# Kernel optimization log

Hardware: AMD Instinct MI355X
Metric: run time of the kernel (lower is better)

Reference implementation:

```python
import jax, jax.numpy as jnp
import numpy as np

N, T, D_FEAT, H = 8192, 60, 6, 64
NEG_SLOPE = 0.01  # torch LeakyReLU default


def setup_inputs() -> dict:
    key = jax.random.key(0)
    ks = jax.random.split(key, 20)
    s = lambda k, shape, fan: jax.random.normal(k, shape, jnp.float32) * (1.0 / np.sqrt(fan))
    inp = {
        'x': jax.random.normal(ks[0], (N, T, D_FEAT), jnp.float32),
        # LSTM layer 0 (input D_FEAT) and layer 1 (input H); gate order i,f,g,o
        'Wih0': s(ks[1], (4 * H, D_FEAT), H), 'Whh0': s(ks[2], (4 * H, H), H),
        'bih0': s(ks[3], (4 * H,), H), 'bhh0': s(ks[4], (4 * H,), H),
        'Wih1': s(ks[5], (4 * H, H), H), 'Whh1': s(ks[6], (4 * H, H), H),
        'bih1': s(ks[7], (4 * H,), H), 'bhh1': s(ks[8], (4 * H,), H),
        # GAT layer: transformation Linear(H,H) and attention vector a [2H,1] (randn in torch)
        'Wt': s(ks[9], (H, H), H), 'bt': s(ks[10], (H,), H),
        'a': jax.random.normal(ks[11], (2 * H, 1), jnp.float32),
        # fc and fc_out
        'Wfc': s(ks[12], (H, H), H), 'bfc': s(ks[13], (H,), H),
        'Wout': s(ks[14], (1, H), H), 'bout': s(ks[15], (1,), H),
    }
    return inp


def _lstm_layer(x, Wih, Whh, bih, bhh):
    # x: [N, T, Din] -> outputs [N, T, H]
    xg = jnp.einsum('ntd,gd->ntg', x, Wih) + bih + bhh  # precompute input gates

    def step(carry, xt):
        h, c = carry
        gates = xt + h @ Whh.T  # [N, 4H]
        i, f, g, o = jnp.split(gates, 4, axis=-1)
        c = jax.nn.sigmoid(f) * c + jax.nn.sigmoid(i) * jnp.tanh(g)
        h = jax.nn.sigmoid(o) * jnp.tanh(c)
        return (h, c), h

    n = x.shape[0]
    h0 = jnp.zeros((n, Whh.shape[1]), x.dtype)
    (_, _), hs = jax.lax.scan(step, (h0, h0), jnp.swapaxes(xg, 0, 1))
    return jnp.swapaxes(hs, 0, 1)


def _gat_layer(x, Wt, bt, a):
    # att[i,j] = leaky_relu(a1 . Wx_j + a2 . Wx_i); softmax over j; out = att @ x
    h = x @ Wt.T + bt                    # [N, H]
    hdim = h.shape[1]
    s1 = (h @ a[:hdim]).squeeze(-1)      # a1 . Wx_j  -> column term
    s2 = (h @ a[hdim:]).squeeze(-1)      # a2 . Wx_i  -> row term
    scores = jax.nn.leaky_relu(s2[:, None] + s1[None, :], NEG_SLOPE)  # [N, N]
    att = jax.nn.softmax(scores, axis=1)
    return att @ x


def reference(x, Wih0, Whh0, bih0, bhh0, Wih1, Whh1, bih1, bhh1,
              Wt, bt, a, Wfc, bfc, Wout, bout):
    out = _lstm_layer(x, Wih0, Whh0, bih0, bhh0)
    out = _lstm_layer(out, Wih1, Whh1, bih1, bhh1)
    last = out[:, -1, :]                 # [N, H]
    hidden = _gat_layer(last, Wt, bt, a) + last  # num_layers_gat = 1
    hidden = jax.nn.leaky_relu(hidden @ Wfc.T + bfc, NEG_SLOPE)
    return (hidden @ Wout.T + bout).squeeze(-1)  # [N]
```

## Files before the change

### kernel.cpp

```cpp
#include <hip/hip_runtime.h>

#define NN 8192
#define TT 60
#define DF 6
#define HH 64
#define GG 256
#define RS 132
#define CH 32
#define NB 256

typedef _Float16 half8 __attribute__((ext_vector_type(8)));
typedef float f32x4 __attribute__((ext_vector_type(4)));
#define MFMA16(a, b, c) __builtin_amdgcn_mfma_f32_16x16x32_f16((a), (b), (c), 0, 0, 0)

#define LOG2E 1.44269504f

__device__ __forceinline__ float lrelu_(float x) { return x > 0.0f ? x : 0.01f * x; }

__device__ __forceinline__ float lstm_act2(float gi, float gf, float gg, float go,
                                           float& c)
{
    const float ei = __builtin_amdgcn_exp2f(gi * -LOG2E);
    const float ef = __builtin_amdgcn_exp2f(gf * -LOG2E);
    const float eg = __builtin_amdgcn_exp2f(fminf(gg * (-2.f * LOG2E), 63.f));
    const float sf = __builtin_amdgcn_rcpf(1.f + ef);
    const float tg_si = (1.f - eg) * __builtin_amdgcn_rcpf((1.f + ei) * (1.f + eg));
    c = __builtin_fmaf(sf, c, tg_si);
    const float eo = __builtin_amdgcn_exp2f(go * -LOG2E);
    const float ec = __builtin_amdgcn_exp2f(fminf(c * (-2.f * LOG2E), 63.f));
    return (1.f - ec) * __builtin_amdgcn_rcpf((1.f + eo) * (1.f + ec));
}

__device__ __forceinline__ half8 ldw8(const float* __restrict__ p) {
    const float4* q = (const float4*)p;
    float4 u = q[0], v = q[1];
    half8 r;
    r[0]=(_Float16)u.x; r[1]=(_Float16)u.y; r[2]=(_Float16)u.z; r[3]=(_Float16)u.w;
    r[4]=(_Float16)v.x; r[5]=(_Float16)v.y; r[6]=(_Float16)v.z; r[7]=(_Float16)v.w;
    return r;
}

#define SXW (TT * 8 + 8)

__global__ __launch_bounds__(512, 4)
void lstm_fused_kernel(const float* __restrict__ x,
                       const float* __restrict__ Wih0, const float* __restrict__ Whh0,
                       const float* __restrict__ bih0, const float* __restrict__ bhh0,
                       const float* __restrict__ Wih1, const float* __restrict__ Whh1,
                       const float* __restrict__ bih1, const float* __restrict__ bhh1,
                       const float* __restrict__ Wt, const float* __restrict__ bt,
                       const float* __restrict__ av,
                       float* __restrict__ last_out,
                       float* __restrict__ s1g, float* __restrict__ s2g)
{
    __shared__ _Float16 sxp[16][SXW];
    __shared__ _Float16 h0buf[2][16][72];
    __shared__ _Float16 h1buf[2][16][72];
    __shared__ _Float16 zero16[8];
    __shared__ float sv1[HH], sv2[HH], sc12[2];

    const int tid  = threadIdx.x;
    const int w    = tid >> 6;
    const int grp  = w >> 2;
    const int cg   = w & 3;
    const int lane = tid & 63;
    const int quad = lane >> 4;
    const int l15  = lane & 15;
    const int hc   = cg * 16 + l15;
    const int n0   = blockIdx.x * 16;

    for (int i = tid; i < 16 * SXW / 2; i += 512) ((unsigned*)sxp)[i] = 0u;
    for (int i = tid; i < 2 * 16 * 72 / 2; i += 512) ((unsigned*)h0buf)[i] = 0u;
    for (int i = tid; i < 2 * 16 * 72 / 2; i += 512) ((unsigned*)h1buf)[i] = 0u;
    if (tid < 4) ((unsigned*)zero16)[tid] = 0u;
    __syncthreads();

    for (int idx = tid; idx < 16 * TT * DF; idx += 512) {
        const int m = idx / (TT * DF);
        const int r = idx - m * (TT * DF);
        const int t = r / DF;
        const int d = r - t * DF;
        sxp[m][t * 8 + d] = (_Float16)x[(size_t)(n0 + m) * (TT * DF) + r];
    }

    if (tid < HH) {
        float a1 = 0.f, a2 = 0.f;
        #pragma unroll 8
        for (int h = 0; h < HH; h++) {
            const float wt = Wt[h * HH + tid];
            a1 += wt * av[h];
            a2 += wt * av[HH + h];
        }
        sv1[tid] = a1; sv2[tid] = a2;
    } else if (tid == 64 || tid == 65) {
        const float* ap = av + (tid - 64) * HH;
        float c = 0.f;
        #pragma unroll 8
        for (int h = 0; h < HH; h++) c += bt[h] * ap[h];
        sc12[tid - 64] = c;
    }

    half8 wA[4][2], wB[4][2];
    float bias[4];
    half8 hzero;
    #pragma unroll
    for (int j = 0; j < 8; j++) hzero[j] = (_Float16)0.f;

    if (grp == 0) {
        #pragma unroll
        for (int nt = 0; nt < 4; nt++) {
            const int g = nt * 64 + hc;
            wA[nt][0] = ldw8(Whh0 + (size_t)g * HH + quad * 8);
            wA[nt][1] = ldw8(Whh0 + (size_t)g * HH + 32 + quad * 8);
            bias[nt]  = bih0[g] + bhh0[g];
            half8 t = hzero;
            if (quad == 0) {
                #pragma unroll
                for (int j = 0; j < DF; j++) t[j] = (_Float16)Wih0[g * DF + j];
            }
            wB[nt][0] = t;
            wB[nt][1] = hzero;
        }
    } else {
        #pragma unroll
        for (int nt = 0; nt < 4; nt++) {
            const int g = nt * 64 + hc;
            wA[nt][0] = ldw8(Wih1 + (size_t)g * HH + quad * 8);
            wA[nt][1] = ldw8(Wih1 + (size_t)g * HH + 32 + quad * 8);
            wB[nt][0] = ldw8(Whh1 + (size_t)g * HH + quad * 8);
            wB[nt][1] = ldw8(Whh1 + (size_t)g * HH + 32 + quad * 8);
            bias[nt]  = bih1[g] + bhh1[g];
        }
    }

    float cs[4] = {0.f, 0.f, 0.f, 0.f};
    __syncthreads();

    for (int i = 0; i <= TT; i++) {
        const int p = i & 1;
        if (grp == 0) {
            if (i < TT) {
                const half8 a0 = *(const half8*)&h0buf[p][l15][quad * 8];
                const half8 a1 = *(const half8*)&h0buf[p][l15][32 + quad * 8];
                const _Float16* xap = (quad == 0) ? &sxp[l15][i * 8] : zero16;
                const half8 ax = *(const half8*)xap;
                f32x4 gv[4];
                #pragma unroll
                for (int nt = 0; nt < 4; nt++) {
                    f32x4 c; c[0] = bias[nt]; c[1] = bias[nt]; c[2] = bias[nt]; c[3] = bias[nt];
                    c = MFMA16(ax, wB[nt][0], c);
                    c = MFMA16(a0, wA[nt][0], c);
                    c = MFMA16(a1, wA[nt][1], c);
                    gv[nt] = c;
                }
                _Float16 (*h0w)[72] = h0buf[p ^ 1];
                #pragma unroll
                for (int reg = 0; reg < 4; reg++) {
                    const float hv = lstm_act2(gv[0][reg], gv[1][reg], gv[2][reg], gv[3][reg], cs[reg]);
                    h0w[quad * 4 + reg][hc] = (_Float16)hv;
                }
            }
        } else {
            if (i > 0) {
                const half8 a00 = *(const half8*)&h0buf[p][l15][quad * 8];
                const half8 a01 = *(const half8*)&h0buf[p][l15][32 + quad * 8];
                const half8 a10 = *(const half8*)&h1buf[p][l15][quad * 8];
                const half8 a11 = *(const half8*)&h1buf[p][l15][32 + quad * 8];
                f32x4 gv[4];
                #pragma unroll
                for (int nt = 0; nt < 4; nt++) {
                    f32x4 c; c[0] = bias[nt]; c[1] = bias[nt]; c[2] = bias[nt]; c[3] = bias[nt];
                    c = MFMA16(a00, wA[nt][0], c);
                    c = MFMA16(a01, wA[nt][1], c);
                    c = MFMA16(a10, wB[nt][0], c);
                    c = MFMA16(a11, wB[nt][1], c);
                    gv[nt] = c;
                }
                _Float16 (*h1w)[72] = h1buf[p ^ 1];
                #pragma unroll
                for (int reg = 0; reg < 4; reg++) {
                    const float hv = lstm_act2(gv[0][reg], gv[1][reg], gv[2][reg], gv[3][reg], cs[reg]);
                    h1w[quad * 4 + reg][hc] = (_Float16)hv;
                    if (i == TT) last_out[(size_t)(n0 + quad * 4 + reg) * HH + hc] = hv;
                }
            }
        }
        __syncthreads();
    }

    {
        const _Float16 (*hf)[72] = h1buf[1];
        const int r  = tid >> 5;
        const int c0 = tid & 31;
        const float h1a = (float)hf[r][c0];
        const float h1b = (float)hf[r][c0 + 32];
        float p1 = h1a * sv1[c0] + h1b * sv1[c0 + 32];
        float p2 = h1a * sv2[c0] + h1b * sv2[c0 + 32];
        #pragma unroll
        for (int off = 16; off > 0; off >>= 1) {
            p1 += __shfl_xor(p1, off);
            p2 += __shfl_xor(p2, off);
        }
        if (c0 == 0) {
            s1g[n0 + r] = p1 + sc12[0];
            s2g[n0 + r] = p2 + sc12[1];
        }
    }
}

__global__ __launch_bounds__(1024)
void rankfac_kernel(const float* __restrict__ s1g, const float* __restrict__ s2g,
                    float* __restrict__ Z, float* __restrict__ Ai, float* __restrict__ Bi,
                    float* __restrict__ U, float* __restrict__ W,
                    int* __restrict__ iperm, float* __restrict__ sortedD)
{
    __shared__ float sb[NN];
    __shared__ float sredw[16];
    __shared__ int   sRank[32];
    const int tid  = threadIdx.x;
    const int lane = tid & 63;
    const int wv   = tid >> 6;
    const int b    = blockIdx.x;
    const int j0   = b * 32;

    {
        const float4* g4 = (const float4*)s1g;
        float4* s4 = (float4*)sb;
        for (int idx = tid; idx < NN / 4; idx += 1024) s4[idx] = g4[idx];
    }
    if (tid < 32) sRank[tid] = 0;
    __syncthreads();

    float m = -1e30f;
    for (int idx = tid; idx < NN; idx += 1024) m = fmaxf(m, sb[idx]);
    #pragma unroll
    for (int off = 32; off > 0; off >>= 1) m = fmaxf(m, __shfl_xor(m, off));
    if (lane == 0) sredw[wv] = m;
    __syncthreads();
    if (tid == 0) {
        float mm = sredw[0];
        #pragma unroll
        for (int q = 1; q < 16; q++) mm = fmaxf(mm, sredw[q]);
        sredw[0] = mm;
    }
    __syncthreads();
    const float s1max = sredw[0];

    if (tid < 32) {
        const int j = j0 + tid;
        const float z  = s2g[j] + s1max;
        const float mi = lrelu_(z);
        Z[j]  = z;
        Ai[j] = __expf(z - mi);
        Bi[j] = __expf(0.01f * z - mi);
        const float d = sb[j] - s1max;
        U[j] = __expf(d);
        W[j] = __expf(0.01f * d);
    }
    {
        const int jl = tid & 31;
        const int part = tid >> 5;
        const float sj = sb[j0 + jl];
        const int jg = j0 + jl;
        const int k0 = part * (NN / 32);
        const float4* sb4 = (const float4*)&sb[k0];
        int cnt = 0;
        #pragma unroll 8
        for (int it = 0; it < NN / 32 / 4; it++) {
            const float4 v = sb4[it];
            const int kb = k0 + it * 4;
            cnt += (v.x < sj || (v.x == sj && kb + 0 < jg)) ? 1 : 0;
            cnt += (v.y < sj || (v.y == sj && kb + 1 < jg)) ? 1 : 0;
            cnt += (v.z < sj || (v.z == sj && kb + 2 < jg)) ? 1 : 0;
            cnt += (v.w < sj || (v.w == sj && kb + 3 < jg)) ? 1 : 0;
        }
        atomicAdd(&sRank[jl], cnt);
    }
    __syncthreads();
    if (tid < 32) {
        const int r = sRank[tid];
        iperm[r] = j0 + tid;
        sortedD[r] = sb[j0 + tid] - s1max;
    }
}

__global__ __launch_bounds__(256)
void scanA_kernel(const float* __restrict__ last, const float* __restrict__ U,
                  const float* __restrict__ W, const int* __restrict__ iperm,
                  float* __restrict__ chunkSum)
{
    __shared__ int   sj[CH];
    __shared__ float su[CH], sw[CH];
    __shared__ float al[CH][HH], bl[CH][HH];
    const int tid = threadIdx.x;
    const int b   = blockIdx.x;
    if (tid < CH) {
        const int j = iperm[b * CH + tid];
        sj[tid] = j; su[tid] = U[j]; sw[tid] = W[j];
    }
    __syncthreads();
    for (int idx = tid; idx < CH * HH; idx += 256) {
        const int rr = idx >> 6, c = idx & 63;
        const float lv = last[(size_t)sj[rr] * HH + c];
        al[rr][c] = su[rr] * lv;
        bl[rr][c] = sw[rr] * lv;
    }
    __syncthreads();
    if (tid < 130) {
        const int c = tid;
        float s = 0.f;
        if (c < 64) {
            for (int rr = 0; rr < CH; rr++) s += al[rr][c];
        } else if (c < 128) {
            for (int rr = 0; rr < CH; rr++) s += bl[rr][c - 64];
        } else if (c == 128) {
            for (int rr = 0; rr < CH; rr++) s += su[rr];
        } else {
            for (int rr = 0; rr < CH; rr++) s += sw[rr];
        }
        chunkSum[b * RS + c] = s;
    }
}

__global__ __launch_bounds__(1024)
void scanC_kernel(const float* __restrict__ last, const float* __restrict__ U,
                  const float* __restrict__ W, const int* __restrict__ iperm,
                  const float* __restrict__ chunkSum, float* __restrict__ PP)
{
    __shared__ int   sj[CH];
    __shared__ float su[CH], sw[CH];
    __shared__ float al[CH][HH], bl[CH][HH];
    __shared__ float pref[130][4];
    const int tid = threadIdx.x;
    const int b   = blockIdx.x;
    if (tid < CH) {
        const int j = iperm[b * CH + tid];
        sj[tid] = j; su[tid] = U[j]; sw[tid] = W[j];
    }
    __syncthreads();
    for (int idx = tid; idx < CH * HH; idx += 1024) {
        const int rr = idx >> 6, c = idx & 63;
        const float lv = last[(size_t)sj[rr] * HH + c];
        al[rr][c] = su[rr] * lv;
        bl[rr][c] = sw[rr] * lv;
    }
    {
        const int c   = tid >> 2;
        const int seg = tid & 3;
        if (c < 130) {
            const bool rev = (c < 64) || (c == 128);
            const int k0 = seg * (NB / 4);
            float s = 0.f;
            #pragma unroll 8
            for (int k = k0; k < k0 + NB / 4; k++) {
                const bool take = rev ? (k > b) : (k < b);
                s += take ? chunkSum[k * RS + c] : 0.f;
            }
            pref[c][seg] = s;
        }
    }
    __syncthreads();
    if (tid < 130) {
        const int c = tid;
        const bool rev = (c < 64) || (c == 128);
        float run = (pref[c][0] + pref[c][1]) + (pref[c][2] + pref[c][3]);
        if (rev) {
            if (b == NB - 1) PP[(size_t)NN * RS + c] = 0.f;
            for (int rr = CH - 1; rr >= 0; rr--) {
                const float val = (c < 64) ? al[rr][c] : su[rr];
                run += val;
                PP[(size_t)(b * CH + rr) * RS + c] = run;
            }
        } else {
            for (int rr = 0; rr < CH; rr++) {
                PP[(size_t)(b * CH + rr) * RS + c] = run;
                run += (c < 128) ? bl[rr][c - 64] : sw[rr];
            }
            if (b == NB - 1) PP[(size_t)NN * RS + c] = run;
        }
    }
}

__global__ __launch_bounds__(256)
void applyfc_kernel(const float* __restrict__ last,
                    const float* __restrict__ Z, const float* __restrict__ Ai, const float* __restrict__ Bi,
                    const float* __restrict__ sortedD, const float* __restrict__ PP,
                    const float* __restrict__ Wfc, const float* __restrict__ bfc,
                    const float* __restrict__ Wout, const float* __restrict__ bout,
                    float* __restrict__ out)
{
    __shared__ float sdD[NN];
    __shared__ float sW[HH][HH + 1];
    __shared__ float sbF[HH], saF[HH];
    const int tid = threadIdx.x;
    {
        const float4* g4 = (const float4*)sortedD;
        float4* s4 = (float4*)sdD;
        for (int idx = tid; idx < NN / 4; idx += 256) s4[idx] = g4[idx];
    }
    for (int idx = tid; idx < HH * HH; idx += 256) {
        const int h = idx >> 6, d = idx & 63;
        sW[d][h] = Wfc[idx];
    }
    if (tid < HH) { sbF[tid] = bfc[tid]; saF[tid] = Wout[tid]; }
    __syncthreads();

    const int wv = tid >> 6, lane = tid & 63;
    const int i0 = blockIdx.x * 16 + wv * 4;
    float zi[4]; int lo[4], hi[4];
    #pragma unroll
    for (int q = 0; q < 4; q++) { zi[q] = Z[i0 + q]; lo[q] = 0; hi[q] = NN; }
    for (int iter = 0; iter < 13; iter++) {
        #pragma unroll
        for (int q = 0; q < 4; q++) {
            if (lo[q] < hi[q]) {
                const int mid = (lo[q] + hi[q]) >> 1;
                const float dm = sdD[mid];
                if (zi[q] + dm > 0.f) hi[q] = mid; else lo[q] = mid + 1;
            }
        }
    }
    float gv[4];
    #pragma unroll
    for (int q = 0; q < 4; q++) {
        const int i = i0 + q;
        const float* rowp = PP + (size_t)lo[q] * RS;
        const float pu  = rowp[lane];
        const float pw  = rowp[64 + lane];
        const float pud = rowp[128];
        const float pwd = rowp[129];
        const float ai = Ai[i], bi = Bi[i];
        const float numer = bi * pw + ai * pu;
        const float den   = bi * pwd + ai * pud;
        const float lv = last[(size_t)i * HH + lane];
        gv[q] = numer * __builtin_amdgcn_rcpf(den) + lv;
    }
    const float bo = bout[0];
    #pragma unroll
    for (int q = 0; q < 4; q++) {
        float acc = sbF[lane];
        #pragma unroll
        for (int d = 0; d < HH; d++) acc += __shfl(gv[q], d) * sW[d][lane];
        float prod = lrelu_(acc) * saF[lane];
        #pragma unroll
        for (int off = 32; off > 0; off >>= 1) prod += __shfl_xor(prod, off);
        if (lane == 0) out[i0 + q] = prod + bo;
    }
}

extern "C" void kernel_launch(void* const* d_in, const int* in_sizes, int n_in,
                              void* d_out, int out_size, void* d_ws, size_t ws_size,
                              hipStream_t stream)
{
    (void)in_sizes; (void)n_in; (void)out_size; (void)ws_size;
    const float* x    = (const float*)d_in[0];
    const float* Wih0 = (const float*)d_in[1];
    const float* Whh0 = (const float*)d_in[2];
    const float* bih0 = (const float*)d_in[3];
    const float* bhh0 = (const float*)d_in[4];
    const float* Wih1 = (const float*)d_in[5];
    const float* Whh1 = (const float*)d_in[6];
    const float* bih1 = (const float*)d_in[7];
    const float* bhh1 = (const float*)d_in[8];
    const float* Wt   = (const float*)d_in[9];
    const float* bt   = (const float*)d_in[10];
    const float* a    = (const float*)d_in[11];
    const float* Wfc  = (const float*)d_in[12];
    const float* bfc  = (const float*)d_in[13];
    const float* Wout = (const float*)d_in[14];
    const float* bout = (const float*)d_in[15];
    float* out = (float*)d_out;

    float* ws       = (float*)d_ws;
    float* last     = ws;
    float* s1g      = last + (size_t)NN*HH;
    float* s2g      = s1g + NN;
    float* Z        = s2g + NN;
    float* Ai       = Z + NN;
    float* Bi       = Ai + NN;
    float* U        = Bi + NN;
    float* W        = U + NN;
    float* sortedD  = W + NN;
    int*   iperm    = (int*)(sortedD + NN);
    float* chunkSum = (float*)(iperm + NN);
    float* chunkOfs = chunkSum + NB*RS;
    float* PP       = chunkOfs + NB*RS;

    lstm_fused_kernel<<<dim3(NN / 16), dim3(512), 0, stream>>>(
        x, Wih0, Whh0, bih0, bhh0, Wih1, Whh1, bih1, bhh1,
        Wt, bt, a, last, s1g, s2g);
    rankfac_kernel<<<dim3(NB), dim3(1024), 0, stream>>>(
        s1g, s2g, Z, Ai, Bi, U, W, iperm, sortedD);
    scanA_kernel<<<dim3(NB), dim3(256), 0, stream>>>(last, U, W, iperm, chunkSum);
    scanC_kernel<<<dim3(NB), dim3(1024), 0, stream>>>(last, U, W, iperm, chunkSum, PP);
    applyfc_kernel<<<dim3(NN / 16), dim3(256), 0, stream>>>(
        last, Z, Ai, Bi, sortedD, PP, Wfc, bfc, Wout, bout, out);
}
```

Measured before the change: 235.1 us.

## Fold activation exp scales into LSTM weights; drop LDS staging of sorted keys

Pre-multiplies the LSTM weights and biases by -log2e (or -2·log2e for the g gate) when loading them, so the per-step activations call exp2 directly without a multiply. Separately, the fc/apply kernel no longer copies the 32 KB sorted array into shared memory per block and instead does the binary search straight from global memory. This trims VALU work in the serial recurrence and cuts per-block LDS fill and footprint, which may raise occupancy. The trade-offs are extra fp16 rounding error from scaling weights before conversion and uncached global loads during the search.

```diff
diff --git a/kernel.cpp b/kernel.cpp
--- a/kernel.cpp
+++ b/kernel.cpp
@@ -17,26 +17,26 @@
 
 __device__ __forceinline__ float lrelu_(float x) { return x > 0.0f ? x : 0.01f * x; }
 
-__device__ __forceinline__ float lstm_act2(float gi, float gf, float gg, float go,
-                                           float& c)
-{
-    const float ei = __builtin_amdgcn_exp2f(gi * -LOG2E);
-    const float ef = __builtin_amdgcn_exp2f(gf * -LOG2E);
-    const float eg = __builtin_amdgcn_exp2f(fminf(gg * (-2.f * LOG2E), 63.f));
+__device__ __forceinline__ float lstm_act2s(float gi, float gf, float gg, float go,
+                                            float& c)
+{
+    const float ei = __builtin_amdgcn_exp2f(gi);
+    const float ef = __builtin_amdgcn_exp2f(gf);
+    const float eg = __builtin_amdgcn_exp2f(fminf(gg, 63.f));
     const float sf = __builtin_amdgcn_rcpf(1.f + ef);
     const float tg_si = (1.f - eg) * __builtin_amdgcn_rcpf((1.f + ei) * (1.f + eg));
     c = __builtin_fmaf(sf, c, tg_si);
-    const float eo = __builtin_amdgcn_exp2f(go * -LOG2E);
+    const float eo = __builtin_amdgcn_exp2f(go);
     const float ec = __builtin_amdgcn_exp2f(fminf(c * (-2.f * LOG2E), 63.f));
     return (1.f - ec) * __builtin_amdgcn_rcpf((1.f + eo) * (1.f + ec));
 }
 
-__device__ __forceinline__ half8 ldw8(const float* __restrict__ p) {
+__device__ __forceinline__ half8 ldw8s(const float* __restrict__ p, float s) {
     const float4* q = (const float4*)p;
     float4 u = q[0], v = q[1];
     half8 r;
-    r[0]=(_Float16)u.x; r[1]=(_Float16)u.y; r[2]=(_Float16)u.z; r[3]=(_Float16)u.w;
-    r[4]=(_Float16)v.x; r[5]=(_Float16)v.y; r[6]=(_Float16)v.z; r[7]=(_Float16)v.w;
+    r[0]=(_Float16)(u.x*s); r[1]=(_Float16)(u.y*s); r[2]=(_Float16)(u.z*s); r[3]=(_Float16)(u.w*s);
+    r[4]=(_Float16)(v.x*s); r[5]=(_Float16)(v.y*s); r[6]=(_Float16)(v.z*s); r[7]=(_Float16)(v.w*s);
     return r;
 }
 
@@ -109,14 +109,15 @@
     if (grp == 0) {
         #pragma unroll
         for (int nt = 0; nt < 4; nt++) {
+            const float sc = (nt == 2) ? (-2.f * LOG2E) : (-LOG2E);
             const int g = nt * 64 + hc;
-            wA[nt][0] = ldw8(Whh0 + (size_t)g * HH + quad * 8);
-            wA[nt][1] = ldw8(Whh0 + (size_t)g * HH + 32 + quad * 8);
-            bias[nt]  = bih0[g] + bhh0[g];
+            wA[nt][0] = ldw8s(Whh0 + (size_t)g * HH + quad * 8, sc);
+            wA[nt][1] = ldw8s(Whh0 + (size_t)g * HH + 32 + quad * 8, sc);
+            bias[nt]  = (bih0[g] + bhh0[g]) * sc;
             half8 t = hzero;
             if (quad == 0) {
                 #pragma unroll
-                for (int j = 0; j < DF; j++) t[j] = (_Float16)Wih0[g * DF + j];
+                for (int j = 0; j < DF; j++) t[j] = (_Float16)(Wih0[g * DF + j] * sc);
             }
             wB[nt][0] = t;
             wB[nt][1] = hzero;
@@ -124,12 +125,13 @@
     } else {
         #pragma unroll
         for (int nt = 0; nt < 4; nt++) {
+            const float sc = (nt == 2) ? (-2.f * LOG2E) : (-LOG2E);
             const int g = nt * 64 + hc;
-            wA[nt][0] = ldw8(Wih1 + (size_t)g * HH + quad * 8);
-            wA[nt][1] = ldw8(Wih1 + (size_t)g * HH + 32 + quad * 8);
-            wB[nt][0] = ldw8(Whh1 + (size_t)g * HH + quad * 8);
-            wB[nt][1] = ldw8(Whh1 + (size_t)g * HH + 32 + quad * 8);
-            bias[nt]  = bih1[g] + bhh1[g];
+            wA[nt][0] = ldw8s(Wih1 + (size_t)g * HH + quad * 8, sc);
+            wA[nt][1] = ldw8s(Wih1 + (size_t)g * HH + 32 + quad * 8, sc);
+            wB[nt][0] = ldw8s(Whh1 + (size_t)g * HH + quad * 8, sc);
+            wB[nt][1] = ldw8s(Whh1 + (size_t)g * HH + 32 + quad * 8, sc);
+            bias[nt]  = (bih1[g] + bhh1[g]) * sc;
         }
     }
 
@@ -156,7 +158,7 @@
                 _Float16 (*h0w)[72] = h0buf[p ^ 1];
                 #pragma unroll
                 for (int reg = 0; reg < 4; reg++) {
-                    const float hv = lstm_act2(gv[0][reg], gv[1][reg], gv[2][reg], gv[3][reg], cs[reg]);
+                    const float hv = lstm_act2s(gv[0][reg], gv[1][reg], gv[2][reg], gv[3][reg], cs[reg]);
                     h0w[quad * 4 + reg][hc] = (_Float16)hv;
                 }
             }
@@ -179,7 +181,7 @@
                 _Float16 (*h1w)[72] = h1buf[p ^ 1];
                 #pragma unroll
                 for (int reg = 0; reg < 4; reg++) {
-                    const float hv = lstm_act2(gv[0][reg], gv[1][reg], gv[2][reg], gv[3][reg], cs[reg]);
+                    const float hv = lstm_act2s(gv[0][reg], gv[1][reg], gv[2][reg], gv[3][reg], cs[reg]);
                     h1w[quad * 4 + reg][hc] = (_Float16)hv;
                     if (i == TT) last_out[(size_t)(n0 + quad * 4 + reg) * HH + hc] = hv;
                 }
@@ -389,15 +391,9 @@
                     const float* __restrict__ Wout, const float* __restrict__ bout,
                     float* __restrict__ out)
 {
-    __shared__ float sdD[NN];
     __shared__ float sW[HH][HH + 1];
     __shared__ float sbF[HH], saF[HH];
     const int tid = threadIdx.x;
-    {
-        const float4* g4 = (const float4*)sortedD;
-        float4* s4 = (float4*)sdD;
-        for (int idx = tid; idx < NN / 4; idx += 256) s4[idx] = g4[idx];
-    }
     for (int idx = tid; idx < HH * HH; idx += 256) {
         const int h = idx >> 6, d = idx & 63;
         sW[d][h] = Wfc[idx];
@@ -415,7 +411,7 @@
         for (int q = 0; q < 4; q++) {
             if (lo[q] < hi[q]) {
                 const int mid = (lo[q] + hi[q]) >> 1;
-                const float dm = sdD[mid];
+                const float dm = sortedD[mid];
                 if (zi[q] + dm > 0.f) hi[q] = mid; else lo[q] = mid + 1;
             }
         }
```

After: 237.6 us. Within noise of the previous version (+1.0%).
